# Performance work log

Hardware: AMD Instinct MI355X
Metric: run time of the kernel (lower is better)

Reference implementation:

```python
import jax, jax.numpy as jnp
import numpy as np

I, H = 16, 32  # input_size, hidden_size


def _rnn_layer(x, W_ih, W_hh, b_ih, b_hh):
    # x: [B, T, D] -> outputs [B, T, H] of tanh RNN layer
    B, T, _ = x.shape
    # precompute input projection for all timesteps: [B, T, H]
    xp = jnp.einsum('btd,hd->bth', x, W_ih) + b_ih + b_hh

    def step(h, xpt):
        h = jnp.tanh(xpt + h @ W_hh.T)
        return h, h

    h0 = jnp.zeros((B, H), dtype=x.dtype)
    _, ys = jax.lax.scan(step, h0, jnp.swapaxes(xp, 0, 1))  # ys: [T, B, H]
    return jnp.swapaxes(ys, 0, 1)


def setup_inputs() -> dict:
    key = jax.random.key(0)
    ks = jax.random.split(key, 11)
    B, T = 4096, 512
    s0 = 1.0 / np.sqrt(H)  # PyTorch RNN init bound
    u = lambda k, shape: jax.random.uniform(k, shape, jnp.float32, -s0, s0)
    return {
        'x': jax.random.normal(ks[0], (B, T, I), jnp.float32),
        'W_ih0': u(ks[1], (H, I)), 'W_hh0': u(ks[2], (H, H)),
        'b_ih0': u(ks[3], (H,)), 'b_hh0': u(ks[4], (H,)),
        'W_ih1': u(ks[5], (H, H)), 'W_hh1': u(ks[6], (H, H)),
        'b_ih1': u(ks[7], (H,)), 'b_hh1': u(ks[8], (H,)),
        'fc_w': u(ks[9], (1, H)), 'fc_b': u(ks[10], (1,)),
    }


def reference(x, W_ih0, W_hh0, b_ih0, b_hh0, W_ih1, W_hh1, b_ih1, b_hh1, fc_w, fc_b):
    h1 = _rnn_layer(x, W_ih0, W_hh0, b_ih0, b_hh0)   # [B, T, H]
    h2 = _rnn_layer(h1, W_ih1, W_hh1, b_ih1, b_hh1)  # [B, T, H]
    last = h2[:, -1, :]                               # [B, H]
    logits = last @ fc_w.T + fc_b                     # [B, 1]
    return logits
```

## Files before the change

kernel.cpp:

```cpp
#include <hip/hip_runtime.h>

#define T_DIM 512
#define I_DIM 16
#define B_DIM 4096
#define K_CH 32
#define COLS 8
#define SCL 2.885390081777927f

typedef _Float16 f16x8 __attribute__((ext_vector_type(8)));
typedef float f32x4 __attribute__((ext_vector_type(4)));
typedef __fp16 hf2v __attribute__((ext_vector_type(2)));

union Frag { f16x8 v; __fp16 e[8]; uint4 u; };

__device__ __forceinline__ float tanh_s(float u) {
    float e = __builtin_amdgcn_exp2f(u);
    return fmaf(-2.f, __builtin_amdgcn_rcpf(e + 1.f), 1.f);
}

__device__ __forceinline__ f16x8 pack8(float a0, float a1, float a2, float a3,
                                       float b0, float b1, float b2, float b3) {
    Frag f;
    hf2v p0 = __builtin_amdgcn_cvt_pkrtz(a0, a1);
    hf2v p1 = __builtin_amdgcn_cvt_pkrtz(a2, a3);
    hf2v p2 = __builtin_amdgcn_cvt_pkrtz(b0, b1);
    hf2v p3 = __builtin_amdgcn_cvt_pkrtz(b2, b3);
    f.e[0] = p0[0]; f.e[1] = p0[1]; f.e[2] = p1[0]; f.e[3] = p1[1];
    f.e[4] = p2[0]; f.e[5] = p2[1]; f.e[6] = p3[0]; f.e[7] = p3[1];
    return f.v;
}
__device__ __forceinline__ f16x8 tanhpack_s(f32x4 a, f32x4 b) {
    return pack8(tanh_s(a[0]), tanh_s(a[1]), tanh_s(a[2]), tanh_s(a[3]),
                 tanh_s(b[0]), tanh_s(b[1]), tanh_s(b[2]), tanh_s(b[3]));
}
__device__ __forceinline__ f16x8 loadWq32s(const float* W, int row, int g) {
    float4 a = *reinterpret_cast<const float4*>(W + row * 32 + 4 * g);
    float4 b = *reinterpret_cast<const float4*>(W + row * 32 + 16 + 4 * g);
    return pack8(a.x*SCL, a.y*SCL, a.z*SCL, a.w*SCL, b.x*SCL, b.y*SCL, b.z*SCL, b.w*SCL);
}
__device__ __forceinline__ f16x8 loadWq16s(const float* W, int row, int g) {
    float4 a = *reinterpret_cast<const float4*>(W + row * 16 + 4 * g);
    return pack8(a.x*SCL, a.y*SCL, a.z*SCL, a.w*SCL, 0.f, 0.f, 0.f, 0.f);
}

__global__ void __launch_bounds__(128)
rnn2_pc8_kernel(const float* __restrict__ x,
                const float* __restrict__ Wih0, const float* __restrict__ Whh0,
                const float* __restrict__ bih0, const float* __restrict__ bhh0,
                const float* __restrict__ Wih1, const float* __restrict__ Whh1,
                const float* __restrict__ bih1, const float* __restrict__ bhh1,
                const float* __restrict__ fcw, const float* __restrict__ fcb,
                float* __restrict__ out)
{
    const int tid = threadIdx.x;
    const int l   = tid & 63;
    const int wid = tid >> 6;
    const int c   = l & 15;
    const int g   = l >> 4;
    const int rowbase = blockIdx.x * COLS;

    __shared__ __fp16 ring[2][K_CH][64][8];

    f16x8 wT0[2], wT1[2];
    f32x4 bC[2];
    Frag  h1f;
    f32x4 Xacc[2];
    float4 xp0, xp1, xp2, xp3, xp4, xp5, xp6, xp7;
    const float* xlane = nullptr;
    float h20=0.f,h21=0.f,h22=0.f,h23=0.f,h24=0.f,h25=0.f,h26=0.f,h27=0.f;
    Frag h2f; h2f.u = make_uint4(0u, 0u, 0u, 0u);

    if (wid == 0) {
#pragma unroll
        for (int tt = 0; tt < 2; ++tt) {
            const int row = c + 16 * tt;
            wT0[tt] = loadWq32s(Whh0, row, g);
            wT1[tt] = loadWq16s(Wih0, row, g);
            const int r0 = 4 * g + 16 * tt;
            float4 bi = *reinterpret_cast<const float4*>(bih0 + r0);
            float4 bh = *reinterpret_cast<const float4*>(bhh0 + r0);
            bC[tt][0] = (bi.x + bh.x) * SCL; bC[tt][1] = (bi.y + bh.y) * SCL;
            bC[tt][2] = (bi.z + bh.z) * SCL; bC[tt][3] = (bi.w + bh.w) * SCL;
        }
        const size_t xcol = rowbase + (c & (COLS - 1));
        xlane = x + xcol * (size_t)(T_DIM * I_DIM) + 4 * g;
    } else {
#pragma unroll
        for (int tt = 0; tt < 2; ++tt) {
            const int row = c + 16 * tt;
            wT0[tt] = loadWq32s(Wih1, row, g);
            wT1[tt] = loadWq32s(Whh1, row, g);
            const int r0 = 4 * g + 16 * tt;
            float4 bi = *reinterpret_cast<const float4*>(bih1 + r0);
            float4 bh = *reinterpret_cast<const float4*>(bhh1 + r0);
            bC[tt][0] = (bi.x + bh.x) * SCL; bC[tt][1] = (bi.y + bh.y) * SCL;
            bC[tt][2] = (bi.z + bh.z) * SCL; bC[tt][3] = (bi.w + bh.w) * SCL;
        }
    }

#define PSTEP(t, P)                                                                         \
    {                                                                                       \
        f32x4 D0a = __builtin_amdgcn_mfma_f32_16x16x32_f16(wT0[0], h1f.v, Xacc[0], 0,0,0);  \
        f32x4 D0b = __builtin_amdgcn_mfma_f32_16x16x32_f16(wT0[1], h1f.v, Xacc[1], 0,0,0);  \
        Frag xf; xf.v = pack8((P).x, (P).y, (P).z, (P).w, 0.f, 0.f, 0.f, 0.f);              \
        const int tn = ((t) + 9 < T_DIM) ? (t) + 9 : (T_DIM - 1);                           \
        (P) = *reinterpret_cast<const float4*>(xlane + (size_t)tn * I_DIM);                 \
        h1f.v = tanhpack_s(D0a, D0b);                                                       \
        *reinterpret_cast<uint4*>(&ring[((t) / K_CH) & 1][(t) & (K_CH - 1)][l][0]) = h1f.u; \
        Xacc[0] = __builtin_amdgcn_mfma_f32_16x16x32_f16(wT1[0], xf.v, bC[0], 0,0,0);       \
        Xacc[1] = __builtin_amdgcn_mfma_f32_16x16x32_f16(wT1[1], xf.v, bC[1], 0,0,0);       \
    }

#pragma unroll 1
    for (int p = 0; p <= T_DIM / K_CH; ++p) {
        if (wid == 0 && p < T_DIM / K_CH) {
            if (p == 0) {
                {
                    float4 xq = *reinterpret_cast<const float4*>(xlane + 0 * I_DIM);
                    Frag xg; xg.v = pack8(xq.x, xq.y, xq.z, xq.w, 0.f, 0.f, 0.f, 0.f);
                    f32x4 A0 = __builtin_amdgcn_mfma_f32_16x16x32_f16(wT1[0], xg.v, bC[0], 0,0,0);
                    f32x4 A1 = __builtin_amdgcn_mfma_f32_16x16x32_f16(wT1[1], xg.v, bC[1], 0,0,0);
                    h1f.v = tanhpack_s(A0, A1);
                    *reinterpret_cast<uint4*>(&ring[0][0][l][0]) = h1f.u;
                }
#pragma unroll
                for (int t = 1; t < 8; ++t) {
                    float4 xq = *reinterpret_cast<const float4*>(xlane + (size_t)t * I_DIM);
                    Frag xg; xg.v = pack8(xq.x, xq.y, xq.z, xq.w, 0.f, 0.f, 0.f, 0.f);
                    f32x4 X0 = __builtin_amdgcn_mfma_f32_16x16x32_f16(wT1[0], xg.v, bC[0], 0,0,0);
                    f32x4 X1 = __builtin_amdgcn_mfma_f32_16x16x32_f16(wT1[1], xg.v, bC[1], 0,0,0);
                    f32x4 D0 = __builtin_amdgcn_mfma_f32_16x16x32_f16(wT0[0], h1f.v, X0, 0,0,0);
                    f32x4 D1 = __builtin_amdgcn_mfma_f32_16x16x32_f16(wT0[1], h1f.v, X1, 0,0,0);
                    h1f.v = tanhpack_s(D0, D1);
                    *reinterpret_cast<uint4*>(&ring[0][t][l][0]) = h1f.u;
                }
                {
                    float4 xq = *reinterpret_cast<const float4*>(xlane + 8 * I_DIM);
                    Frag xg; xg.v = pack8(xq.x, xq.y, xq.z, xq.w, 0.f, 0.f, 0.f, 0.f);
                    Xacc[0] = __builtin_amdgcn_mfma_f32_16x16x32_f16(wT1[0], xg.v, bC[0], 0,0,0);
                    Xacc[1] = __builtin_amdgcn_mfma_f32_16x16x32_f16(wT1[1], xg.v, bC[1], 0,0,0);
                }
                xp0 = *reinterpret_cast<const float4*>(xlane +  9 * I_DIM);
                xp1 = *reinterpret_cast<const float4*>(xlane + 10 * I_DIM);
                xp2 = *reinterpret_cast<const float4*>(xlane + 11 * I_DIM);
                xp3 = *reinterpret_cast<const float4*>(xlane + 12 * I_DIM);
                xp4 = *reinterpret_cast<const float4*>(xlane + 13 * I_DIM);
                xp5 = *reinterpret_cast<const float4*>(xlane + 14 * I_DIM);
                xp6 = *reinterpret_cast<const float4*>(xlane + 15 * I_DIM);
                xp7 = *reinterpret_cast<const float4*>(xlane + 16 * I_DIM);
#pragma unroll 1
                for (int sgrp = 8; sgrp < K_CH; sgrp += 8) {
                    PSTEP(sgrp + 0, xp0) PSTEP(sgrp + 1, xp1)
                    PSTEP(sgrp + 2, xp2) PSTEP(sgrp + 3, xp3)
                    PSTEP(sgrp + 4, xp4) PSTEP(sgrp + 5, xp5)
                    PSTEP(sgrp + 6, xp6) PSTEP(sgrp + 7, xp7)
                }
            } else {
                const int t0 = p * K_CH;
#pragma unroll 1
                for (int sgrp = 0; sgrp < K_CH; sgrp += 8) {
                    PSTEP(t0 + sgrp + 0, xp0) PSTEP(t0 + sgrp + 1, xp1)
                    PSTEP(t0 + sgrp + 2, xp2) PSTEP(t0 + sgrp + 3, xp3)
                    PSTEP(t0 + sgrp + 4, xp4) PSTEP(t0 + sgrp + 5, xp5)
                    PSTEP(t0 + sgrp + 6, xp6) PSTEP(t0 + sgrp + 7, xp7)
                }
            }
        }
        if (wid == 1 && p >= 1) {
            const int cp  = p - 1;
            const int buf = cp & 1;
            Frag hB; hB.u = *reinterpret_cast<const uint4*>(&ring[buf][0][l][0]);
            f32x4 pd1a = __builtin_amdgcn_mfma_f32_16x16x32_f16(wT0[0], hB.v, bC[0], 0,0,0);
            f32x4 pd1b = __builtin_amdgcn_mfma_f32_16x16x32_f16(wT0[1], hB.v, bC[1], 0,0,0);
#pragma unroll 2
            for (int s = 0; s < K_CH; ++s) {
                f32x4 D1a = __builtin_amdgcn_mfma_f32_16x16x32_f16(wT1[0], h2f.v, pd1a, 0,0,0);
                f32x4 D1b = __builtin_amdgcn_mfma_f32_16x16x32_f16(wT1[1], h2f.v, pd1b, 0,0,0);
                const int sn = (s + 1 < K_CH) ? s + 1 : s;
                hB.u = *reinterpret_cast<const uint4*>(&ring[buf][sn][l][0]);
                pd1a = __builtin_amdgcn_mfma_f32_16x16x32_f16(wT0[0], hB.v, bC[0], 0,0,0);
                pd1b = __builtin_amdgcn_mfma_f32_16x16x32_f16(wT0[1], hB.v, bC[1], 0,0,0);
                h20 = tanh_s(D1a[0]); h21 = tanh_s(D1a[1]);
                h22 = tanh_s(D1a[2]); h23 = tanh_s(D1a[3]);
                h24 = tanh_s(D1b[0]); h25 = tanh_s(D1b[1]);
                h26 = tanh_s(D1b[2]); h27 = tanh_s(D1b[3]);
                h2f.v = pack8(h20, h21, h22, h23, h24, h25, h26, h27);
            }
        }
        __syncthreads();
    }
#undef PSTEP

    if (wid == 1) {
        float4 fw0 = *reinterpret_cast<const float4*>(fcw + 4 * g);
        float4 fw1 = *reinterpret_cast<const float4*>(fcw + 16 + 4 * g);
        float part = fw0.x * h20 + fw0.y * h21 + fw0.z * h22 + fw0.w * h23
                   + fw1.x * h24 + fw1.y * h25 + fw1.z * h26 + fw1.w * h27;
        part += __shfl_xor(part, 16, 64);
        part += __shfl_xor(part, 32, 64);
        if (l < COLS) out[rowbase + l] = part + fcb[0];
    }
}

extern "C" void kernel_launch(void* const* d_in, const int* in_sizes, int n_in,
                              void* d_out, int out_size, void* d_ws, size_t ws_size,
                              hipStream_t stream) {
    const float* x    = (const float*)d_in[0];
    const float* Wih0 = (const float*)d_in[1];
    const float* Whh0 = (const float*)d_in[2];
    const float* bih0 = (const float*)d_in[3];
    const float* bhh0 = (const float*)d_in[4];
    const float* Wih1 = (const float*)d_in[5];
    const float* Whh1 = (const float*)d_in[6];
    const float* bih1 = (const float*)d_in[7];
    const float* bhh1 = (const float*)d_in[8];
    const float* fcw  = (const float*)d_in[9];
    const float* fcb  = (const float*)d_in[10];
    float* out = (float*)d_out;

    dim3 grid(B_DIM / COLS);
    rnn2_pc8_kernel<<<grid, 128, 0, stream>>>(x, Wih0, Whh0, bih0, bhh0,
                                              Wih1, Whh1, bih1, bhh1,
                                              fcw, fcb, out);
}
```

Baseline: 91.92 us.

## Move layer-1 input projection into producer wave and halve chunk size

The layer-0 wave now also computes the layer-1 input projection (W_ih1·h1 + bias) right after each tanh. It writes fp32 pre-activations to shared memory, so the layer-1 wave only does the recurrent matmul and tanh on its serial path. The chunk size drops from 32 to 16 steps, which shortens pipeline fill and drain, and the producer loop is fully unrolled. The cost is more MFMA work and twice the LDS traffic on the producer wave, plus twice as many block barriers.

```diff
diff --git a/kernel.cpp b/kernel.cpp
--- a/kernel.cpp
+++ b/kernel.cpp
@@ -3,7 +3,8 @@
 #define T_DIM 512
 #define I_DIM 16
 #define B_DIM 4096
-#define K_CH 32
+#define K_CH 16
+#define NCH  (T_DIM / K_CH)
 #define COLS 8
 #define SCL 2.885390081777927f
 
@@ -44,7 +45,7 @@
 }
 
 __global__ void __launch_bounds__(128)
-rnn2_pc8_kernel(const float* __restrict__ x,
+rnn2_pd1_kernel(const float* __restrict__ x,
                 const float* __restrict__ Wih0, const float* __restrict__ Whh0,
                 const float* __restrict__ bih0, const float* __restrict__ bhh0,
                 const float* __restrict__ Wih1, const float* __restrict__ Whh1,
@@ -59,10 +60,10 @@
     const int g   = l >> 4;
     const int rowbase = blockIdx.x * COLS;
 
-    __shared__ __fp16 ring[2][K_CH][64][8];
-
-    f16x8 wT0[2], wT1[2];
-    f32x4 bC[2];
+    __shared__ float ring[2][K_CH][2][64][4];
+
+    f16x8 wHH[2], wIH1[2], wIH0[2];
+    f32x4 b0C[2], b1C[2];
     Frag  h1f;
     f32x4 Xacc[2];
     float4 xp0, xp1, xp2, xp3, xp4, xp5, xp6, xp7;
@@ -74,71 +75,71 @@
 #pragma unroll
         for (int tt = 0; tt < 2; ++tt) {
             const int row = c + 16 * tt;
-            wT0[tt] = loadWq32s(Whh0, row, g);
-            wT1[tt] = loadWq16s(Wih0, row, g);
+            wHH[tt]  = loadWq32s(Whh0, row, g);
+            wIH0[tt] = loadWq16s(Wih0, row, g);
+            wIH1[tt] = loadWq32s(Wih1, row, g);
             const int r0 = 4 * g + 16 * tt;
-            float4 bi = *reinterpret_cast<const float4*>(bih0 + r0);
-            float4 bh = *reinterpret_cast<const float4*>(bhh0 + r0);
-            bC[tt][0] = (bi.x + bh.x) * SCL; bC[tt][1] = (bi.y + bh.y) * SCL;
-            bC[tt][2] = (bi.z + bh.z) * SCL; bC[tt][3] = (bi.w + bh.w) * SCL;
+            float4 bi0 = *reinterpret_cast<const float4*>(bih0 + r0);
+            float4 bh0 = *reinterpret_cast<const float4*>(bhh0 + r0);
+            b0C[tt][0] = (bi0.x + bh0.x) * SCL; b0C[tt][1] = (bi0.y + bh0.y) * SCL;
+            b0C[tt][2] = (bi0.z + bh0.z) * SCL; b0C[tt][3] = (bi0.w + bh0.w) * SCL;
+            float4 bi1 = *reinterpret_cast<const float4*>(bih1 + r0);
+            float4 bh1 = *reinterpret_cast<const float4*>(bhh1 + r0);
+            b1C[tt][0] = (bi1.x + bh1.x) * SCL; b1C[tt][1] = (bi1.y + bh1.y) * SCL;
+            b1C[tt][2] = (bi1.z + bh1.z) * SCL; b1C[tt][3] = (bi1.w + bh1.w) * SCL;
         }
         const size_t xcol = rowbase + (c & (COLS - 1));
         xlane = x + xcol * (size_t)(T_DIM * I_DIM) + 4 * g;
     } else {
 #pragma unroll
         for (int tt = 0; tt < 2; ++tt) {
-            const int row = c + 16 * tt;
-            wT0[tt] = loadWq32s(Wih1, row, g);
-            wT1[tt] = loadWq32s(Whh1, row, g);
-            const int r0 = 4 * g + 16 * tt;
-            float4 bi = *reinterpret_cast<const float4*>(bih1 + r0);
-            float4 bh = *reinterpret_cast<const float4*>(bhh1 + r0);
-            bC[tt][0] = (bi.x + bh.x) * SCL; bC[tt][1] = (bi.y + bh.y) * SCL;
-            bC[tt][2] = (bi.z + bh.z) * SCL; bC[tt][3] = (bi.w + bh.w) * SCL;
+            wHH[tt] = loadWq32s(Whh1, c + 16 * tt, g);
         }
     }
 
 #define PSTEP(t, P)                                                                         \
     {                                                                                       \
-        f32x4 D0a = __builtin_amdgcn_mfma_f32_16x16x32_f16(wT0[0], h1f.v, Xacc[0], 0,0,0);  \
-        f32x4 D0b = __builtin_amdgcn_mfma_f32_16x16x32_f16(wT0[1], h1f.v, Xacc[1], 0,0,0);  \
+        f32x4 D0a = __builtin_amdgcn_mfma_f32_16x16x32_f16(wHH[0], h1f.v, Xacc[0], 0,0,0);  \
+        f32x4 D0b = __builtin_amdgcn_mfma_f32_16x16x32_f16(wHH[1], h1f.v, Xacc[1], 0,0,0);  \
         Frag xf; xf.v = pack8((P).x, (P).y, (P).z, (P).w, 0.f, 0.f, 0.f, 0.f);              \
         const int tn = ((t) + 9 < T_DIM) ? (t) + 9 : (T_DIM - 1);                           \
         (P) = *reinterpret_cast<const float4*>(xlane + (size_t)tn * I_DIM);                 \
         h1f.v = tanhpack_s(D0a, D0b);                                                       \
-        *reinterpret_cast<uint4*>(&ring[((t) / K_CH) & 1][(t) & (K_CH - 1)][l][0]) = h1f.u; \
-        Xacc[0] = __builtin_amdgcn_mfma_f32_16x16x32_f16(wT1[0], xf.v, bC[0], 0,0,0);       \
-        Xacc[1] = __builtin_amdgcn_mfma_f32_16x16x32_f16(wT1[1], xf.v, bC[1], 0,0,0);       \
+        f32x4 pa = __builtin_amdgcn_mfma_f32_16x16x32_f16(wIH1[0], h1f.v, b1C[0], 0,0,0);   \
+        f32x4 pb = __builtin_amdgcn_mfma_f32_16x16x32_f16(wIH1[1], h1f.v, b1C[1], 0,0,0);   \
+        *reinterpret_cast<f32x4*>(&ring[((t) / K_CH) & 1][(t) & (K_CH - 1)][0][l][0]) = pa; \
+        *reinterpret_cast<f32x4*>(&ring[((t) / K_CH) & 1][(t) & (K_CH - 1)][1][l][0]) = pb; \
+        Xacc[0] = __builtin_amdgcn_mfma_f32_16x16x32_f16(wIH0[0], xf.v, b0C[0], 0,0,0);     \
+        Xacc[1] = __builtin_amdgcn_mfma_f32_16x16x32_f16(wIH0[1], xf.v, b0C[1], 0,0,0);     \
     }
 
 #pragma unroll 1
-    for (int p = 0; p <= T_DIM / K_CH; ++p) {
-        if (wid == 0 && p < T_DIM / K_CH) {
+    for (int p = 0; p <= NCH; ++p) {
+        if (wid == 0 && p < NCH) {
             if (p == 0) {
-                {
-                    float4 xq = *reinterpret_cast<const float4*>(xlane + 0 * I_DIM);
-                    Frag xg; xg.v = pack8(xq.x, xq.y, xq.z, xq.w, 0.f, 0.f, 0.f, 0.f);
-                    f32x4 A0 = __builtin_amdgcn_mfma_f32_16x16x32_f16(wT1[0], xg.v, bC[0], 0,0,0);
-                    f32x4 A1 = __builtin_amdgcn_mfma_f32_16x16x32_f16(wT1[1], xg.v, bC[1], 0,0,0);
-                    h1f.v = tanhpack_s(A0, A1);
-                    *reinterpret_cast<uint4*>(&ring[0][0][l][0]) = h1f.u;
-                }
 #pragma unroll
-                for (int t = 1; t < 8; ++t) {
+                for (int t = 0; t < 8; ++t) {
                     float4 xq = *reinterpret_cast<const float4*>(xlane + (size_t)t * I_DIM);
                     Frag xg; xg.v = pack8(xq.x, xq.y, xq.z, xq.w, 0.f, 0.f, 0.f, 0.f);
-                    f32x4 X0 = __builtin_amdgcn_mfma_f32_16x16x32_f16(wT1[0], xg.v, bC[0], 0,0,0);
-                    f32x4 X1 = __builtin_amdgcn_mfma_f32_16x16x32_f16(wT1[1], xg.v, bC[1], 0,0,0);
-                    f32x4 D0 = __builtin_amdgcn_mfma_f32_16x16x32_f16(wT0[0], h1f.v, X0, 0,0,0);
-                    f32x4 D1 = __builtin_amdgcn_mfma_f32_16x16x32_f16(wT0[1], h1f.v, X1, 0,0,0);
+                    f32x4 X0 = __builtin_amdgcn_mfma_f32_16x16x32_f16(wIH0[0], xg.v, b0C[0], 0,0,0);
+                    f32x4 X1 = __builtin_amdgcn_mfma_f32_16x16x32_f16(wIH0[1], xg.v, b0C[1], 0,0,0);
+                    f32x4 D0, D1;
+                    if (t == 0) { D0 = X0; D1 = X1; }
+                    else {
+                        D0 = __builtin_amdgcn_mfma_f32_16x16x32_f16(wHH[0], h1f.v, X0, 0,0,0);
+                        D1 = __builtin_amdgcn_mfma_f32_16x16x32_f16(wHH[1], h1f.v, X1, 0,0,0);
+                    }
                     h1f.v = tanhpack_s(D0, D1);
-                    *reinterpret_cast<uint4*>(&ring[0][t][l][0]) = h1f.u;
+                    f32x4 pa = __builtin_amdgcn_mfma_f32_16x16x32_f16(wIH1[0], h1f.v, b1C[0], 0,0,0);
+                    f32x4 pb = __builtin_amdgcn_mfma_f32_16x16x32_f16(wIH1[1], h1f.v, b1C[1], 0,0,0);
+                    *reinterpret_cast<f32x4*>(&ring[0][t][0][l][0]) = pa;
+                    *reinterpret_cast<f32x4*>(&ring[0][t][1][l][0]) = pb;
                 }
                 {
                     float4 xq = *reinterpret_cast<const float4*>(xlane + 8 * I_DIM);
                     Frag xg; xg.v = pack8(xq.x, xq.y, xq.z, xq.w, 0.f, 0.f, 0.f, 0.f);
-                    Xacc[0] = __builtin_amdgcn_mfma_f32_16x16x32_f16(wT1[0], xg.v, bC[0], 0,0,0);
-                    Xacc[1] = __builtin_amdgcn_mfma_f32_16x16x32_f16(wT1[1], xg.v, bC[1], 0,0,0);
+                    Xacc[0] = __builtin_amdgcn_mfma_f32_16x16x32_f16(wIH0[0], xg.v, b0C[0], 0,0,0);
+                    Xacc[1] = __builtin_amdgcn_mfma_f32_16x16x32_f16(wIH0[1], xg.v, b0C[1], 0,0,0);
                 }
                 xp0 = *reinterpret_cast<const float4*>(xlane +  9 * I_DIM);
                 xp1 = *reinterpret_cast<const float4*>(xlane + 10 * I_DIM);
@@ -148,38 +149,31 @@
                 xp5 = *reinterpret_cast<const float4*>(xlane + 14 * I_DIM);
                 xp6 = *reinterpret_cast<const float4*>(xlane + 15 * I_DIM);
                 xp7 = *reinterpret_cast<const float4*>(xlane + 16 * I_DIM);
-#pragma unroll 1
-                for (int sgrp = 8; sgrp < K_CH; sgrp += 8) {
-                    PSTEP(sgrp + 0, xp0) PSTEP(sgrp + 1, xp1)
-                    PSTEP(sgrp + 2, xp2) PSTEP(sgrp + 3, xp3)
-                    PSTEP(sgrp + 4, xp4) PSTEP(sgrp + 5, xp5)
-                    PSTEP(sgrp + 6, xp6) PSTEP(sgrp + 7, xp7)
-                }
+                PSTEP( 8, xp0) PSTEP( 9, xp1) PSTEP(10, xp2) PSTEP(11, xp3)
+                PSTEP(12, xp4) PSTEP(13, xp5) PSTEP(14, xp6) PSTEP(15, xp7)
             } else {
                 const int t0 = p * K_CH;
-#pragma unroll 1
-                for (int sgrp = 0; sgrp < K_CH; sgrp += 8) {
-                    PSTEP(t0 + sgrp + 0, xp0) PSTEP(t0 + sgrp + 1, xp1)
-                    PSTEP(t0 + sgrp + 2, xp2) PSTEP(t0 + sgrp + 3, xp3)
-                    PSTEP(t0 + sgrp + 4, xp4) PSTEP(t0 + sgrp + 5, xp5)
-                    PSTEP(t0 + sgrp + 6, xp6) PSTEP(t0 + sgrp + 7, xp7)
-                }
+                PSTEP(t0 +  0, xp0) PSTEP(t0 +  1, xp1)
+                PSTEP(t0 +  2, xp2) PSTEP(t0 +  3, xp3)
+                PSTEP(t0 +  4, xp4) PSTEP(t0 +  5, xp5)
+                PSTEP(t0 +  6, xp6) PSTEP(t0 +  7, xp7)
+                PSTEP(t0 +  8, xp0) PSTEP(t0 +  9, xp1)
+                PSTEP(t0 + 10, xp2) PSTEP(t0 + 11, xp3)
+                PSTEP(t0 + 12, xp4) PSTEP(t0 + 13, xp5)
+                PSTEP(t0 + 14, xp6) PSTEP(t0 + 15, xp7)
             }
         }
         if (wid == 1 && p >= 1) {
-            const int cp  = p - 1;
-            const int buf = cp & 1;
-            Frag hB; hB.u = *reinterpret_cast<const uint4*>(&ring[buf][0][l][0]);
-            f32x4 pd1a = __builtin_amdgcn_mfma_f32_16x16x32_f16(wT0[0], hB.v, bC[0], 0,0,0);
-            f32x4 pd1b = __builtin_amdgcn_mfma_f32_16x16x32_f16(wT0[1], hB.v, bC[1], 0,0,0);
+            const int buf = (p - 1) & 1;
+            f32x4 lda = *reinterpret_cast<const f32x4*>(&ring[buf][0][0][l][0]);
+            f32x4 ldb = *reinterpret_cast<const f32x4*>(&ring[buf][0][1][l][0]);
 #pragma unroll 2
             for (int s = 0; s < K_CH; ++s) {
-                f32x4 D1a = __builtin_amdgcn_mfma_f32_16x16x32_f16(wT1[0], h2f.v, pd1a, 0,0,0);
-                f32x4 D1b = __builtin_amdgcn_mfma_f32_16x16x32_f16(wT1[1], h2f.v, pd1b, 0,0,0);
+                f32x4 D1a = __builtin_amdgcn_mfma_f32_16x16x32_f16(wHH[0], h2f.v, lda, 0,0,0);
+                f32x4 D1b = __builtin_amdgcn_mfma_f32_16x16x32_f16(wHH[1], h2f.v, ldb, 0,0,0);
                 const int sn = (s + 1 < K_CH) ? s + 1 : s;
-                hB.u = *reinterpret_cast<const uint4*>(&ring[buf][sn][l][0]);
-                pd1a = __builtin_amdgcn_mfma_f32_16x16x32_f16(wT0[0], hB.v, bC[0], 0,0,0);
-                pd1b = __builtin_amdgcn_mfma_f32_16x16x32_f16(wT0[1], hB.v, bC[1], 0,0,0);
+                lda = *reinterpret_cast<const f32x4*>(&ring[buf][sn][0][l][0]);
+                ldb = *reinterpret_cast<const f32x4*>(&ring[buf][sn][1][l][0]);
                 h20 = tanh_s(D1a[0]); h21 = tanh_s(D1a[1]);
                 h22 = tanh_s(D1a[2]); h23 = tanh_s(D1a[3]);
                 h24 = tanh_s(D1b[0]); h25 = tanh_s(D1b[1]);
@@ -219,7 +213,7 @@
     float* out = (float*)d_out;
 
     dim3 grid(B_DIM / COLS);
-    rnn2_pc8_kernel<<<grid, 128, 0, stream>>>(x, Wih0, Whh0, bih0, bhh0,
+    rnn2_pd1_kernel<<<grid, 128, 0, stream>>>(x, Wih0, Whh0, bih0, bhh0,
                                               Wih1, Whh1, bih1, bhh1,
                                               fcw, fcb, out);
 }
```

Result: slower. 105.4 us (+14.7%).
